# Performance work log

Hardware: AMD Instinct MI355X
Metric: run time of the kernel (lower is better)

Reference implementation:

```python
import jax, jax.numpy as jnp
import numpy as np

H = 1024          # hidden_size
A = 8             # num_actions
T = 64            # timesteps
N = 256           # batch (num envs)


def _gru_cell(x, h, Wih, Whh, bih, bhh):
    # torch.nn.GRUCell math; gate order (r, z, n)
    gi = x @ Wih.T + bih           # [N, 3H]
    gh = h @ Whh.T + bhh           # [N, 3H]
    i_r, i_z, i_n = jnp.split(gi, 3, axis=1)
    h_r, h_z, h_n = jnp.split(gh, 3, axis=1)
    r = jax.nn.sigmoid(i_r + h_r)
    z = jax.nn.sigmoid(i_z + h_z)
    n = jnp.tanh(i_n + r * h_n)
    return (1.0 - z) * n + z * h


def setup_inputs() -> dict:
    key = jax.random.key(0)
    ks = jax.random.split(key, 12)
    s = 0.02
    return {
        "c": jax.random.normal(ks[0], (T * N, H), jnp.float32),
        "hxs": jax.random.normal(ks[1], (N, 3 * H), jnp.float32),
        "masks": jnp.ones((T * N, 1), jnp.float32),
        "prev_action_one_hot": jnp.zeros((T * N, A), jnp.float32).at[jnp.arange(T * N), jax.random.randint(ks[2], (T * N,), 0, A)].set(1.0),
        "h_gru_Wih": s * jax.random.normal(ks[3], (3 * H, H), jnp.float32),
        "h_gru_Whh": s * jax.random.normal(ks[4], (3 * H, H), jnp.float32),
        "h_gru_bih": jnp.zeros((3 * H,), jnp.float32),
        "h_gru_bhh": jnp.zeros((3 * H,), jnp.float32),
        "f_gru_Wih": s * jax.random.normal(ks[5], (3 * H, H), jnp.float32),
        "f_gru_Whh": s * jax.random.normal(ks[6], (3 * H, H), jnp.float32),
        "f_gru_bih": jnp.zeros((3 * H,), jnp.float32),
        "f_gru_bhh": jnp.zeros((3 * H,), jnp.float32),
        "p_W": s * jax.random.normal(ks[7], (2 * H, 2 * H + A), jnp.float32),
        "p_b": jnp.zeros((2 * H,), jnp.float32),
        "q_W": s * jax.random.normal(ks[8], (2 * H, 2 * H + A), jnp.float32),
        "q_b": jnp.zeros((2 * H,), jnp.float32),
    }


def reference(c, hxs, masks, prev_action_one_hot,
              h_gru_Wih, h_gru_Whh, h_gru_bih, h_gru_bhh,
              f_gru_Wih, f_gru_Whh, f_gru_bih, f_gru_bhh,
              p_W, p_b, q_W, q_b):
    c3 = c.reshape(T, N, H)
    m3 = masks.reshape(T, N, 1)
    a3 = prev_action_one_hot.reshape(T, N, A)
    f0 = hxs[:, :H]
    h0 = hxs[:, H:2 * H]
    q0 = hxs[:, 2 * H:]

    def step(carry, xs):
        f, h, q_mu = carry
        c_t, m_t, a_t = xs
        p_in = jnp.concatenate([h, q_mu, a_t], axis=1) * m_t
        p_dist = p_in @ p_W.T + p_b                     # [N, 2H]
        p_mu = p_dist[:, :H]
        q_in = jnp.concatenate([f, c_t, a_t], axis=1) * m_t
        q_dist = q_in @ q_W.T + q_b                     # [N, 2H]
        q_mu_new = q_dist[:, :H]
        f_new = _gru_cell(c_t, f * m_t, f_gru_Wih, f_gru_Whh, f_gru_bih, f_gru_bhh)
        h_new = _gru_cell(p_mu, h * m_t, h_gru_Wih, h_gru_Whh, h_gru_bih, h_gru_bhh)
        return (f_new, h_new, q_mu_new), (p_dist, q_dist)

    (f, h, q_mu), (p_all, q_all) = jax.lax.scan(step, (f0, h0, q0), (c3, m3, a3))
    acc_p = p_all.reshape(T * N, 2 * H)
    acc_q = q_all.reshape(T * N, 2 * H)
    hxs_out = jnp.concatenate([f, h, q_mu], axis=1)
    return acc_p, acc_q, hxs_out
```

## Files before the change

kernel.cpp:

```cpp
#include <hip/hip_runtime.h>
#include <math.h>

typedef __attribute__((ext_vector_type(8))) __bf16 bf16x8;
typedef __attribute__((ext_vector_type(4))) float f32x4;

constexpr int H = 1024, T = 64, NB = 256, TWOH = 2048, THREEH = 3072;
constexpr long long OFF_Q  = 33554432LL;
constexpr long long OFF_HX = 67108864LL;
constexpr int LA = 6;

constexpr int R_PWH = 0, R_PWQ = 2048, R_QWF = 4096, R_QWC = 6144,
              R_FWIH = 8192, R_FWHH = 11264, R_HWIH = 14336, R_HWHH = 17408;

#define LD4(p) (*reinterpret_cast<const float4*>(p))

__device__ __forceinline__ float sigf(float x) { return 1.0f / (1.0f + expf(-x)); }

__device__ __forceinline__ void gload16(const void* g, void* l) {
    __builtin_amdgcn_global_load_lds(
        (const __attribute__((address_space(1))) uint32_t*)g,
        (__attribute__((address_space(3))) uint32_t*)l, 16, 0, 0);
}

__device__ __forceinline__ void st_bf_swz(__bf16* base, int n, int k, float v) {
    base[(size_t)n * 1024 + (((k >> 3) ^ (n & 7)) << 3) + (k & 7)] = (__bf16)v;
}

#define FRAGOFF(rloc, gl) (((rloc) << 7) + ((((gl)) ^ ((rloc) & 7)) << 4))

template<int RT>
__device__ __forceinline__ void stage_tile(const char* g, char* l, int kb, int tid) {
    #pragma unroll
    for (int i = 0; i < RT / 32; ++i) {
        const int L = i * 4096 + tid * 16;
        gload16(g + (size_t)(L >> 7) * 2048 + (size_t)kb * 128 + (L & 127), l + L);
    }
}

__device__ __forceinline__ void mm128(
    int tid, char* sA, char* sB,
    const char* A, const char* B, int nit,
    f32x4 (&acc)[2][4])
{
    const int lane = tid & 63, w = tid >> 6;
    const int l15 = lane & 15, lg = lane >> 4;
    const int wr = w >> 1, wc = w & 1;
    int aoff[2][2], boff[4][2];
    #pragma unroll
    for (int fr = 0; fr < 2; ++fr)
        #pragma unroll
        for (int kk = 0; kk < 2; ++kk)
            aoff[fr][kk] = FRAGOFF(wr * 32 + fr * 16 + l15, kk * 4 + lg);
    #pragma unroll
    for (int fc = 0; fc < 4; ++fc)
        #pragma unroll
        for (int kk = 0; kk < 2; ++kk)
            boff[fc][kk] = FRAGOFF(wc * 64 + fc * 16 + l15, kk * 4 + lg);

    stage_tile<64>(A, sA, 0, tid);
    stage_tile<128>(B, sB, 0, tid);
    if (nit > 1) {
        stage_tile<64>(A, sA + 8192, 1, tid);
        stage_tile<128>(B, sB + 16384, 1, tid);
    }
    for (int kb = 0; kb < nit; ++kb) {
        const int kn = kb + 2;
        if (kn < nit) {
            const int bo = kn % 3;
            stage_tile<64>(A, sA + bo * 8192, kn, tid);
            stage_tile<128>(B, sB + bo * 16384, kn, tid);
            asm volatile("s_waitcnt vmcnt(12)" ::: "memory");
        } else if (kb + 1 < nit) {
            asm volatile("s_waitcnt vmcnt(6)" ::: "memory");
        } else {
            asm volatile("s_waitcnt vmcnt(0)" ::: "memory");
        }
        __builtin_amdgcn_s_barrier();
        __builtin_amdgcn_sched_barrier(0);
        const int bc = kb % 3;
        char* Ab = sA + bc * 8192;
        char* Bb = sB + bc * 16384;
        bf16x8 af[2][2], bv[4][2];
        #pragma unroll
        for (int fr = 0; fr < 2; ++fr)
            #pragma unroll
            for (int kk = 0; kk < 2; ++kk)
                af[fr][kk] = *reinterpret_cast<const bf16x8*>(Ab + aoff[fr][kk]);
        #pragma unroll
        for (int fc = 0; fc < 4; ++fc)
            #pragma unroll
            for (int kk = 0; kk < 2; ++kk)
                bv[fc][kk] = *reinterpret_cast<const bf16x8*>(Bb + boff[fc][kk]);
        __builtin_amdgcn_s_setprio(1);
        #pragma unroll
        for (int kk = 0; kk < 2; ++kk)
            #pragma unroll
            for (int fr = 0; fr < 2; ++fr)
                #pragma unroll
                for (int fc = 0; fc < 4; ++fc)
                    acc[fr][fc] = __builtin_amdgcn_mfma_f32_16x16x32_bf16(
                        af[fr][kk], bv[fc][kk], acc[fr][fc], 0, 0, 0);
        __builtin_amdgcn_s_setprio(0);
        __builtin_amdgcn_s_barrier();
        __builtin_amdgcn_sched_barrier(0);
    }
}

__device__ __forceinline__ void mm32g1(
    int tid, char* sA, char* sB,
    const char* A, const char* Bg,
    f32x4 (&aR)[2], f32x4 (&aZ)[2], f32x4 (&aN)[2])
{
    const int lane = tid & 63, w = tid >> 6;
    const int l15 = lane & 15, lg = lane >> 4;
    const int wr = w >> 1, wc = w & 1;
    int aoff[2], boff[2][2];
    #pragma unroll
    for (int kk = 0; kk < 2; ++kk)
        aoff[kk] = FRAGOFF(wr * 16 + l15, kk * 4 + lg);
    #pragma unroll
    for (int fc = 0; fc < 2; ++fc)
        #pragma unroll
        for (int kk = 0; kk < 2; ++kk)
            boff[fc][kk] = FRAGOFF(wc * 32 + fc * 16 + l15, kk * 4 + lg);

    auto stg = [&](int buf, int kb) {
        stage_tile<32>(A, sA + buf * 4096, kb, tid);
        #pragma unroll
        for (int g = 0; g < 3; ++g)
            stage_tile<64>(Bg + (size_t)g * 2097152, sB + buf * 24576 + g * 8192, kb, tid);
    };
    stg(0, 0);
    for (int kb = 0; kb < 16; ++kb) {
        if (kb + 1 < 16) {
            stg((kb + 1) & 1, kb + 1);
            asm volatile("s_waitcnt vmcnt(7)" ::: "memory");
        } else {
            asm volatile("s_waitcnt vmcnt(0)" ::: "memory");
        }
        __builtin_amdgcn_s_barrier();
        __builtin_amdgcn_sched_barrier(0);
        char* Ab = sA + (kb & 1) * 4096;
        char* Bb = sB + (kb & 1) * 24576;
        bf16x8 af[2];
        #pragma unroll
        for (int kk = 0; kk < 2; ++kk)
            af[kk] = *reinterpret_cast<const bf16x8*>(Ab + aoff[kk]);
        bf16x8 bvr[2][2], bvz[2][2], bvn[2][2];
        #pragma unroll
        for (int fc = 0; fc < 2; ++fc)
            #pragma unroll
            for (int kk = 0; kk < 2; ++kk) {
                bvr[fc][kk] = *reinterpret_cast<const bf16x8*>(Bb + boff[fc][kk]);
                bvz[fc][kk] = *reinterpret_cast<const bf16x8*>(Bb + 8192 + boff[fc][kk]);
                bvn[fc][kk] = *reinterpret_cast<const bf16x8*>(Bb + 16384 + boff[fc][kk]);
            }
        __builtin_amdgcn_s_setprio(1);
        #pragma unroll
        for (int kk = 0; kk < 2; ++kk)
            #pragma unroll
            for (int fc = 0; fc < 2; ++fc) {
                aR[fc] = __builtin_amdgcn_mfma_f32_16x16x32_bf16(af[kk], bvr[fc][kk], aR[fc], 0, 0, 0);
                aZ[fc] = __builtin_amdgcn_mfma_f32_16x16x32_bf16(af[kk], bvz[fc][kk], aZ[fc], 0, 0, 0);
                aN[fc] = __builtin_amdgcn_mfma_f32_16x16x32_bf16(af[kk], bvn[fc][kk], aN[fc], 0, 0, 0);
            }
        __builtin_amdgcn_s_setprio(0);
        __builtin_amdgcn_s_barrier();
        __builtin_amdgcn_sched_barrier(0);
    }
}

__device__ __forceinline__ void do_xq(int slice, int i, int tid, char* sA, char* sB,
    const char* cbfB, const char* Wb, const float* act, const float* qW, float* out)
{
    const int lane = tid & 63, w = tid >> 6;
    const int l15 = lane & 15, lg = lane >> 4;
    const int wr = w >> 1, wc = w & 1;
    const int row0 = (i >> 4) * 64, col0 = (i & 15) * 128;
    const size_t grow0 = (size_t)slice * NB + row0;
    f32x4 acc[2][4] = {};
    mm128(tid, sA, sB, cbfB + grow0 * 2048, Wb + (size_t)(R_QWC + col0) * 2048, 16, acc);
    #pragma unroll
    for (int fc = 0; fc < 4; ++fc) {
        const int gc = col0 + wc * 64 + fc * 16 + l15;
        const float* wp = qW + (size_t)gc * 2056 + 2048;
        float4 x0 = LD4(wp), x1 = LD4(wp + 4);
        #pragma unroll
        for (int fr = 0; fr < 2; ++fr)
            #pragma unroll
            for (int j = 0; j < 4; ++j) {
                const size_t n = grow0 + wr * 32 + fr * 16 + lg * 4 + j;
                const float* ar = act + n * 8;
                float4 a0 = LD4(ar), a1 = LD4(ar + 4);
                float dot = a0.x * x0.x + a0.y * x0.y + a0.z * x0.z + a0.w * x0.w
                          + a1.x * x1.x + a1.y * x1.y + a1.z * x1.z + a1.w * x1.w;
                out[OFF_Q + n * TWOH + gc] = acc[fr][fc][j] + dot;
            }
    }
}

__device__ __forceinline__ void do_gf(int slice, int i, int tid, char* sA, char* sB,
    const char* cbfB, const char* Wb, __bf16* Gfb)
{
    const int lane = tid & 63, w = tid >> 6;
    const int l15 = lane & 15, lg = lane >> 4;
    const int wr = w >> 1, wc = w & 1;
    const int row0 = (i / 24) * 64, col0 = (i % 24) * 128;
    f32x4 acc[2][4] = {};
    mm128(tid, sA, sB, cbfB + ((size_t)slice * NB + row0) * 2048,
          Wb + (size_t)(R_FWIH + col0) * 2048, 16, acc);
    __bf16* gdst = Gfb + (size_t)(slice & 7) * NB * THREEH;
    #pragma unroll
    for (int fc = 0; fc < 4; ++fc) {
        const int gc = col0 + wc * 64 + fc * 16 + l15;
        #pragma unroll
        for (int fr = 0; fr < 2; ++fr)
            #pragma unroll
            for (int j = 0; j < 4; ++j) {
                const int n = row0 + wr * 32 + fr * 16 + lg * 4 + j;
                gdst[(size_t)n * THREEH + gc] = (__bf16)acc[fr][fc][j];
            }
    }
}

__device__ __forceinline__ void do_pq(int tt, int i, int tid, char* sA, char* sB,
    const __bf16* qmu_t, const char* Wb, const float* masks, const float* act,
    const float* pW, const float* pb, float* out)
{
    const int lane = tid & 63, w = tid >> 6;
    const int l15 = lane & 15, lg = lane >> 4;
    const int wr = w >> 1, wc = w & 1;
    const int row0 = (i >> 4) * 64, col0 = (i & 15) * 128;
    f32x4 acc[2][4] = {};
    mm128(tid, sA, sB, (const char*)qmu_t + (size_t)row0 * 2048,
          Wb + (size_t)(R_PWQ + col0) * 2048, 16, acc);
    const float* mrow = masks + (size_t)tt * NB;
    float* ob = out + (size_t)tt * NB * TWOH;
    #pragma unroll
    for (int fc = 0; fc < 4; ++fc) {
        const int gc = col0 + wc * 64 + fc * 16 + l15;
        const float* wp = pW + (size_t)gc * 2056 + 2048;
        float4 x0 = LD4(wp), x1 = LD4(wp + 4);
        const float bb = pb[gc];
        #pragma unroll
        for (int fr = 0; fr < 2; ++fr)
            #pragma unroll
            for (int j = 0; j < 4; ++j) {
                const int n = row0 + wr * 32 + fr * 16 + lg * 4 + j;
                const float* ar = act + ((size_t)tt * NB + n) * 8;
                float4 a0 = LD4(ar), a1 = LD4(ar + 4);
                float dot = a0.x * x0.x + a0.y * x0.y + a0.z * x0.z + a0.w * x0.w
                          + a1.x * x1.x + a1.y * x1.y + a1.z * x1.z + a1.w * x1.w;
                ob[(size_t)n * TWOH + gc] = acc[fr][fc][j] + mrow[n] * dot + bb;
            }
    }
}

__global__ __launch_bounds__(256) void wcvt_k(
    const float* __restrict__ pW, const float* __restrict__ qW,
    const float* __restrict__ fWih, const float* __restrict__ fWhh,
    const float* __restrict__ hWih, const float* __restrict__ hWhh,
    __bf16* __restrict__ Wbf)
{
    const long i = (long)blockIdx.x * 256 + threadIdx.x;
    const int row = (int)(i >> 7);
    const int G   = (int)i & 127;
    const float* src; int stride; int koff = 0; int r;
    if (row < 2048)       { src = pW;   stride = 2056; koff = 0;    r = row; }
    else if (row < 4096)  { src = pW;   stride = 2056; koff = 1024; r = row - 2048; }
    else if (row < 6144)  { src = qW;   stride = 2056; koff = 0;    r = row - 4096; }
    else if (row < 8192)  { src = qW;   stride = 2056; koff = 1024; r = row - 6144; }
    else if (row < 11264) { src = fWih; stride = 1024; r = row - 8192; }
    else if (row < 14336) { src = fWhh; stride = 1024; r = row - 11264; }
    else if (row < 17408) { src = hWih; stride = 1024; r = row - 14336; }
    else                  { src = hWhh; stride = 1024; r = row - 17408; }
    const float* p = src + (long)r * stride + koff + G * 8;
    float4 a = LD4(p), b = LD4(p + 4);
    bf16x8 v;
    v[0] = (__bf16)a.x; v[1] = (__bf16)a.y; v[2] = (__bf16)a.z; v[3] = (__bf16)a.w;
    v[4] = (__bf16)b.x; v[5] = (__bf16)b.y; v[6] = (__bf16)b.z; v[7] = (__bf16)b.w;
    *reinterpret_cast<bf16x8*>(Wbf + (size_t)row * 1024 + ((G ^ (row & 7)) << 3)) = v;
}

__global__ __launch_bounds__(256) void ccvt_k(const float* __restrict__ c,
                                              __bf16* __restrict__ cbf) {
    const long i = (long)blockIdx.x * 256 + threadIdx.x;
    const int row = (int)(i >> 7);
    const int G   = (int)i & 127;
    const float* p = c + (size_t)row * 1024 + G * 8;
    float4 a = LD4(p), b = LD4(p + 4);
    bf16x8 v;
    v[0] = (__bf16)a.x; v[1] = (__bf16)a.y; v[2] = (__bf16)a.z; v[3] = (__bf16)a.w;
    v[4] = (__bf16)b.x; v[5] = (__bf16)b.y; v[6] = (__bf16)b.z; v[7] = (__bf16)b.w;
    *reinterpret_cast<bf16x8*>(cbf + (size_t)row * 1024 + ((G ^ (row & 7)) << 3)) = v;
}

__global__ __launch_bounds__(256) void init2_k(
    const float* __restrict__ hxs, const float* __restrict__ masks,
    float* __restrict__ fst0, float* __restrict__ hst0,
    __bf16* __restrict__ fbm0, __bf16* __restrict__ hbm0, __bf16* __restrict__ qmub0)
{
    const int idx = blockIdx.x * 256 + threadIdx.x;
    const int arr = idx >> 15;
    const int g   = idx & 32767;
    const int n   = g >> 7;
    const int G   = g & 127;
    const float m0 = masks[n];
    const float* p = hxs + (size_t)n * THREEH + arr * 1024 + G * 8;
    float4 a = LD4(p), b = LD4(p + 4);
    __bf16* dstB = arr == 0 ? fbm0 : (arr == 1 ? hbm0 : qmub0);
    bf16x8 v;
    v[0] = (__bf16)(a.x * m0); v[1] = (__bf16)(a.y * m0);
    v[2] = (__bf16)(a.z * m0); v[3] = (__bf16)(a.w * m0);
    v[4] = (__bf16)(b.x * m0); v[5] = (__bf16)(b.y * m0);
    v[6] = (__bf16)(b.z * m0); v[7] = (__bf16)(b.w * m0);
    *reinterpret_cast<bf16x8*>(dstB + (size_t)n * 1024 + ((G ^ (n & 7)) << 3)) = v;
    if (arr < 2) {
        float* dstF = arr == 0 ? fst0 : hst0;
        *reinterpret_cast<float4*>(dstF + (size_t)n * 1024 + G * 8) = a;
        *reinterpret_cast<float4*>(dstF + (size_t)n * 1024 + G * 8 + 4) = b;
    }
}

__global__ __launch_bounds__(256) void pre_k(
    const char* __restrict__ cbfB, const char* __restrict__ Wb,
    const float* __restrict__ act, const float* __restrict__ qW,
    const __bf16* __restrict__ qmb0, const float* __restrict__ masks,
    const float* __restrict__ pW, const float* __restrict__ pb,
    __bf16* __restrict__ Gfb, float* __restrict__ out)
{
    __shared__ char smem[73728];
    if (blockIdx.x < LA * 160) {
        const int s = blockIdx.x / 160;
        const int i = blockIdx.x % 160;
        if (i < 64) do_xq(s, i, threadIdx.x, smem, smem + 24576, cbfB, Wb, act, qW, out);
        else        do_gf(s, i - 64, threadIdx.x, smem, smem + 24576, cbfB, Wb, Gfb);
    } else {
        do_pq(0, blockIdx.x - LA * 160, threadIdx.x, smem, smem + 24576,
              qmb0, Wb, masks, act, pW, pb, out);
    }
}

__global__ __launch_bounds__(256) void k1_k(
    int t,
    const __bf16* __restrict__ hbm, const __bf16* __restrict__ fbm,
    __bf16* __restrict__ qmubN,
    const float* __restrict__ masks, const float* __restrict__ act,
    const float* __restrict__ qb, const float* __restrict__ qW,
    const char* __restrict__ Wb,
    __bf16* __restrict__ pmub, float* __restrict__ Shh,
    const __bf16* __restrict__ Gfb,
    const float* __restrict__ fbih, const float* __restrict__ fbhh,
    const float* __restrict__ fstF, float* __restrict__ fstN, __bf16* __restrict__ fbmN,
    float* __restrict__ out)
{
    __shared__ char smem[73728];
    char* sA = smem;
    char* sB = smem + 24576;
    const int tid = threadIdx.x;
    const int lane = tid & 63, w = tid >> 6;
    const int l15 = lane & 15, lg = lane >> 4;
    const int wr = w >> 1, wc = w & 1;
    const float* mrow = masks + (size_t)t * NB;
    const float* mn   = masks + (size_t)(t + 1 < T ? t + 1 : t) * NB;
    int b = blockIdx.x;

    if (b < 64) {
        const int row0 = (b >> 4) * 64, col0 = (b & 15) * 128;
        f32x4 acc[2][4] = {};
        mm128(tid, sA, sB,
              (const char*)hbm + (size_t)row0 * 2048,
              Wb + (size_t)(R_PWH + col0) * 2048, 16, acc);
        float* ob = out + (size_t)t * NB * TWOH;
        #pragma unroll
        for (int fc = 0; fc < 4; ++fc) {
            const int gc = col0 + wc * 64 + fc * 16 + l15;
            #pragma unroll
            for (int fr = 0; fr < 2; ++fr)
                #pragma unroll
                for (int j = 0; j < 4; ++j) {
                    const int n = row0 + wr * 32 + fr * 16 + lg * 4 + j;
                    const float v = ob[(size_t)n * TWOH + gc] + acc[fr][fc][j];
                    ob[(size_t)n * TWOH + gc] = v;
                    if (gc < 1024) st_bf_swz(pmub, n, gc, v);
                }
        }
    } else if (b < 128) {
        b -= 64;
        const int row0 = (b >> 4) * 64, col0 = (b & 15) * 128;
        f32x4 acc[2][4] = {};
        mm128(tid, sA, sB,
              (const char*)fbm + (size_t)row0 * 2048,
              Wb + (size_t)(R_QWF + col0) * 2048, 16, acc);
        float* ob = out + OFF_Q + (size_t)t * NB * TWOH;
        #pragma unroll
        for (int fc = 0; fc < 4; ++fc) {
            const int gc = col0 + wc * 64 + fc * 16 + l15;
            const float bb = qb[gc];
            #pragma unroll
            for (int fr = 0; fr < 2; ++fr)
                #pragma unroll
                for (int j = 0; j < 4; ++j) {
                    const int n = row0 + wr * 32 + fr * 16 + lg * 4 + j;
                    const float xq = ob[(size_t)n * TWOH + gc];
                    float v = acc[fr][fc][j] + mrow[n] * xq + bb;
                    ob[(size_t)n * TWOH + gc] = v;
                    if (gc < 1024) st_bf_swz(qmubN, n, gc, v * mn[n]);
                }
        }
    } else if (b < 224) {
        const int i = b - 128;
        const int row0 = (i / 24) * 64, col0 = (i % 24) * 128;
        f32x4 acc[2][4] = {};
        mm128(tid, sA, sB,
              (const char*)hbm + (size_t)row0 * 2048,
              Wb + (size_t)(R_HWHH + col0) * 2048, 16, acc);
        #pragma unroll
        for (int fc = 0; fc < 4; ++fc) {
            const int gc = col0 + wc * 64 + fc * 16 + l15;
            #pragma unroll
            for (int fr = 0; fr < 2; ++fr)
                #pragma unroll
                for (int j = 0; j < 4; ++j) {
                    const int n = row0 + wr * 32 + fr * 16 + lg * 4 + j;
                    Shh[(size_t)n * THREEH + gc] = acc[fr][fc][j];
                }
        }
    } else {
        const int i = b - 224;
        const int row0 = (i >> 4) * 32, col0 = (i & 15) * 64;
        f32x4 aR[2] = {}, aZ[2] = {}, aN[2] = {};
        mm32g1(tid, sA, sB,
               (const char*)fbm + (size_t)row0 * 2048,
               Wb + (size_t)(R_FWHH + col0) * 2048, aR, aZ, aN);
        const __bf16* gsl = Gfb + (size_t)(t & 7) * NB * THREEH;
        #pragma unroll
        for (int fc = 0; fc < 2; ++fc) {
            const int col = col0 + wc * 32 + fc * 16 + l15;
            const float br  = fbih[col] + fbhh[col];
            const float bz  = fbih[col + 1024] + fbhh[col + 1024];
            const float bni = fbih[col + 2048], bnh = fbhh[col + 2048];
            #pragma unroll
            for (int j = 0; j < 4; ++j) {
                const int n = row0 + wr * 16 + lg * 4 + j;
                const float gfr = (float)gsl[(size_t)n * THREEH + col];
                const float gfz = (float)gsl[(size_t)n * THREEH + col + 1024];
                const float gfn = (float)gsl[(size_t)n * THREEH + col + 2048];
                const float rg = sigf(gfr + aR[fc][j] + br);
                const float zg = sigf(gfz + aZ[fc][j] + bz);
                const float ng = tanhf(gfn + bni + rg * (aN[fc][j] + bnh));
                const float fm = fstF[(size_t)n * 1024 + col] * mrow[n];
                const float o = (1.f - zg) * ng + zg * fm;
                fstN[(size_t)n * 1024 + col] = o;
                st_bf_swz(fbmN, n, col, o * mn[n]);
            }
        }
    }
}

__global__ __launch_bounds__(256) void k2_k(
    int t,
    const __bf16* __restrict__ pmub, const __bf16* __restrict__ qmubN,
    const char* __restrict__ cbfB,
    const float* __restrict__ Shh,
    const float* __restrict__ hstF, float* __restrict__ hstN, __bf16* __restrict__ hbmN,
    const char* __restrict__ Wb,
    const float* __restrict__ hbih, const float* __restrict__ hbhh,
    const float* __restrict__ masks, const float* __restrict__ act,
    const float* __restrict__ pW, const float* __restrict__ pb,
    const float* __restrict__ qW,
    __bf16* __restrict__ Gfb, float* __restrict__ out)
{
    __shared__ char smem[73728];
    char* sA = smem;
    char* sB = smem + 24576;
    const int tid = threadIdx.x;
    const int lane = tid & 63, w = tid >> 6;
    const int l15 = lane & 15, lg = lane >> 4;
    const int wr = w >> 1, wc = w & 1;
    const float* mrow = masks + (size_t)t * NB;
    const float* mn   = masks + (size_t)(t + 1 < T ? t + 1 : t) * NB;
    const int b = blockIdx.x;

    if (b < 128) {
        const int row0 = (b >> 4) * 32, col0 = (b & 15) * 64;
        f32x4 aR[2] = {}, aZ[2] = {}, aN[2] = {};
        mm32g1(tid, sA, sB,
               (const char*)pmub + (size_t)row0 * 2048,
               Wb + (size_t)(R_HWIH + col0) * 2048, aR, aZ, aN);
        #pragma unroll
        for (int fc = 0; fc < 2; ++fc) {
            const int col = col0 + wc * 32 + fc * 16 + l15;
            const float bri = hbih[col],        brh = hbhh[col];
            const float bzi = hbih[col + 1024], bzh = hbhh[col + 1024];
            const float bni = hbih[col + 2048], bnh = hbhh[col + 2048];
            #pragma unroll
            for (int j = 0; j < 4; ++j) {
                const int n = row0 + wr * 16 + lg * 4 + j;
                const float ghr = Shh[(size_t)n * THREEH + col];
                const float ghz = Shh[(size_t)n * THREEH + col + 1024];
                const float ghn = Shh[(size_t)n * THREEH + col + 2048];
                const float rg = sigf(aR[fc][j] + bri + ghr + brh);
                const float zg = sigf(aZ[fc][j] + bzi + ghz + bzh);
                const float ng = tanhf(aN[fc][j] + bni + rg * (ghn + bnh));
                const float hm = hstF[(size_t)n * 1024 + col] * mrow[n];
                const float o = (1.f - zg) * ng + zg * hm;
                hstN[(size_t)n * 1024 + col] = o;
                st_bf_swz(hbmN, n, col, o * mn[n]);
            }
        }
    } else if (b < 192) {
        if (t + 1 < T)
            do_pq(t + 1, b - 128, tid, sA, sB, qmubN, Wb, masks, act, pW, pb, out);
    } else if (b < 256) {
        if (t + LA < T)
            do_xq(t + LA, b - 192, tid, sA, sB, cbfB, Wb, act, qW, out);
    } else {
        if (t + LA < T)
            do_gf(t + LA, b - 256, tid, sA, sB, cbfB, Wb, Gfb);
    }
}

__global__ __launch_bounds__(256) void write_hxs_k(const float* __restrict__ fS,
                                                   const float* __restrict__ hS,
                                                   float* out) {
    const int i = blockIdx.x * 256 + threadIdx.x;
    const int n = i / THREEH;
    const int j = i - n * THREEH;
    float v;
    if (j < H)          v = fS[(size_t)n * H + j];
    else if (j < TWOH)  v = hS[(size_t)n * H + (j - H)];
    else                v = out[OFF_Q + ((size_t)(T - 1) * NB + n) * TWOH + (j - TWOH)];
    out[OFF_HX + i] = v;
}

extern "C" void kernel_launch(void* const* d_in, const int* in_sizes, int n_in,
                              void* d_out, int out_size, void* d_ws, size_t ws_size,
                              hipStream_t stream) {
    (void)in_sizes; (void)n_in; (void)out_size; (void)ws_size;

    const float* c     = (const float*)d_in[0];
    const float* hxs   = (const float*)d_in[1];
    const float* masks = (const float*)d_in[2];
    const float* act   = (const float*)d_in[3];
    const float* hWih  = (const float*)d_in[4];
    const float* hWhh  = (const float*)d_in[5];
    const float* hbih  = (const float*)d_in[6];
    const float* hbhh  = (const float*)d_in[7];
    const float* fWih  = (const float*)d_in[8];
    const float* fWhh  = (const float*)d_in[9];
    const float* fbih  = (const float*)d_in[10];
    const float* fbhh  = (const float*)d_in[11];
    const float* pW    = (const float*)d_in[12];
    const float* pb    = (const float*)d_in[13];
    const float* qW    = (const float*)d_in[14];
    const float* qb    = (const float*)d_in[15];

    float* out = (float*)d_out;
    char*  wsb = (char*)d_ws;

    __bf16* Wbf  = (__bf16*)(wsb);
    __bf16* cbf  = (__bf16*)(wsb + 41943040LL);
    float*  fst[2] = { (float*)(wsb + 75497472LL), (float*)(wsb + 76546048LL) };
    float*  hst[2] = { (float*)(wsb + 77594624LL), (float*)(wsb + 78643200LL) };
    __bf16* fbm[2] = { (__bf16*)(wsb + 79691776LL), (__bf16*)(wsb + 80216064LL) };
    __bf16* hbm[2] = { (__bf16*)(wsb + 80740352LL), (__bf16*)(wsb + 81264640LL) };
    __bf16* qmb[2] = { (__bf16*)(wsb + 81788928LL), (__bf16*)(wsb + 82313216LL) };
    __bf16* pmub   = (__bf16*)(wsb + 82837504LL);
    float*  Shh    = (float*)(wsb + 83361792LL);
    __bf16* Gfb    = (__bf16*)(wsb + 86507520LL);
    const char* Wb   = (const char*)Wbf;
    const char* cbfB = (const char*)cbf;

    wcvt_k <<<dim3(10240), dim3(256), 0, stream>>>(pW, qW, fWih, fWhh, hWih, hWhh, Wbf);
    ccvt_k <<<dim3(8192),  dim3(256), 0, stream>>>(c, cbf);
    init2_k<<<dim3(384),   dim3(256), 0, stream>>>(hxs, masks, fst[0], hst[0],
                                                   fbm[0], hbm[0], qmb[0]);
    pre_k  <<<dim3(LA * 160 + 64), dim3(256), 0, stream>>>(
        cbfB, Wb, act, qW, qmb[0], masks, pW, pb, Gfb, out);

    for (int t = 0; t < T; ++t) {
        const int cur = t & 1, nxt = cur ^ 1;
        k1_k<<<dim3(352), dim3(256), 0, stream>>>(
            t, hbm[cur], fbm[cur], qmb[nxt],
            masks, act, qb, qW, Wb, pmub, Shh, Gfb,
            fbih, fbhh, fst[cur], fst[nxt], fbm[nxt], out);
        k2_k<<<dim3(352), dim3(256), 0, stream>>>(
            t, pmub, qmb[nxt], cbfB, Shh,
            hst[cur], hst[nxt], hbm[nxt],
            Wb, hbih, hbhh, masks, act, pW, pb, qW, Gfb, out);
    }

    write_hxs_k<<<dim3(3072), dim3(256), 0, stream>>>(fst[0], hst[0], out);
}
```

Baseline: 2.107 ms.

## Load weight B-fragments straight from global into registers, dropping LDS staging

The GEMM helpers now read weight fragments directly from global memory into a double-buffered register set, using unswizzled weight rows. Only the activation tile still goes through a triple-buffered LDS ring. This shrinks shared memory from 72KB to 24KB per block, which allows more resident blocks and removes LDS write/read traffic for the weights. In exchange it uses more VGPRs and issues uncoalesced-ish per-lane global loads for B, which could expose latency.

```diff
diff --git a/kernel.cpp b/kernel.cpp
--- a/kernel.cpp
+++ b/kernel.cpp
@@ -38,59 +38,56 @@
 }
 
 __device__ __forceinline__ void mm128(
-    int tid, char* sA, char* sB,
-    const char* A, const char* B, int nit,
+    int tid, char* sA,
+    const char* A, const char* B,
     f32x4 (&acc)[2][4])
 {
     const int lane = tid & 63, w = tid >> 6;
     const int l15 = lane & 15, lg = lane >> 4;
     const int wr = w >> 1, wc = w & 1;
-    int aoff[2][2], boff[4][2];
+    int aoff[2][2];
     #pragma unroll
     for (int fr = 0; fr < 2; ++fr)
         #pragma unroll
         for (int kk = 0; kk < 2; ++kk)
             aoff[fr][kk] = FRAGOFF(wr * 32 + fr * 16 + l15, kk * 4 + lg);
+    const char* Bp[4];
     #pragma unroll
     for (int fc = 0; fc < 4; ++fc)
+        Bp[fc] = B + (size_t)(wc * 64 + fc * 16 + l15) * 2048 + (lg << 4);
+
+    bf16x8 br0[4][2], br1[4][2];
+    stage_tile<64>(A, sA, 0, tid);
+    stage_tile<64>(A, sA + 8192, 1, tid);
+    #pragma unroll
+    for (int fc = 0; fc < 4; ++fc)
         #pragma unroll
         for (int kk = 0; kk < 2; ++kk)
-            boff[fc][kk] = FRAGOFF(wc * 64 + fc * 16 + l15, kk * 4 + lg);
-
-    stage_tile<64>(A, sA, 0, tid);
-    stage_tile<128>(B, sB, 0, tid);
-    if (nit > 1) {
-        stage_tile<64>(A, sA + 8192, 1, tid);
-        stage_tile<128>(B, sB + 16384, 1, tid);
-    }
-    for (int kb = 0; kb < nit; ++kb) {
-        const int kn = kb + 2;
-        if (kn < nit) {
-            const int bo = kn % 3;
-            stage_tile<64>(A, sA + bo * 8192, kn, tid);
-            stage_tile<128>(B, sB + bo * 16384, kn, tid);
-            asm volatile("s_waitcnt vmcnt(12)" ::: "memory");
-        } else if (kb + 1 < nit) {
-            asm volatile("s_waitcnt vmcnt(6)" ::: "memory");
-        } else {
-            asm volatile("s_waitcnt vmcnt(0)" ::: "memory");
-        }
+            br0[fc][kk] = *reinterpret_cast<const bf16x8*>(Bp[fc] + kk * 64);
+
+    auto step = [&](int kb, bf16x8 (&bc)[4][2], bf16x8 (&bw)[4][2]) {
+        if (kb + 2 < 16)
+            stage_tile<64>(A, sA + ((kb + 2) % 3) * 8192, kb + 2, tid);
+        if (kb + 1 < 16) {
+            #pragma unroll
+            for (int fc = 0; fc < 4; ++fc)
+                #pragma unroll
+                for (int kk = 0; kk < 2; ++kk)
+                    bw[fc][kk] = *reinterpret_cast<const bf16x8*>(
+                        Bp[fc] + (kb + 1) * 128 + kk * 64);
+        }
+        if (kb + 2 < 16)      asm volatile("s_waitcnt vmcnt(10)" ::: "memory");
+        else if (kb + 1 < 16) asm volatile("s_waitcnt vmcnt(8)" ::: "memory");
+        else                  asm volatile("s_waitcnt vmcnt(0)" ::: "memory");
         __builtin_amdgcn_s_barrier();
         __builtin_amdgcn_sched_barrier(0);
-        const int bc = kb % 3;
-        char* Ab = sA + bc * 8192;
-        char* Bb = sB + bc * 16384;
-        bf16x8 af[2][2], bv[4][2];
+        char* Ab = sA + (kb % 3) * 8192;
+        bf16x8 af[2][2];
         #pragma unroll
         for (int fr = 0; fr < 2; ++fr)
             #pragma unroll
             for (int kk = 0; kk < 2; ++kk)
                 af[fr][kk] = *reinterpret_cast<const bf16x8*>(Ab + aoff[fr][kk]);
-        #pragma unroll
-        for (int fc = 0; fc < 4; ++fc)
-            #pragma unroll
-            for (int kk = 0; kk < 2; ++kk)
-                bv[fc][kk] = *reinterpret_cast<const bf16x8*>(Bb + boff[fc][kk]);
         __builtin_amdgcn_s_setprio(1);
         #pragma unroll
         for (int kk = 0; kk < 2; ++kk)
@@ -99,78 +96,93 @@
                 #pragma unroll
                 for (int fc = 0; fc < 4; ++fc)
                     acc[fr][fc] = __builtin_amdgcn_mfma_f32_16x16x32_bf16(
-                        af[fr][kk], bv[fc][kk], acc[fr][fc], 0, 0, 0);
+                        af[fr][kk], bc[fc][kk], acc[fr][fc], 0, 0, 0);
         __builtin_amdgcn_s_setprio(0);
         __builtin_amdgcn_s_barrier();
         __builtin_amdgcn_sched_barrier(0);
+    };
+    #pragma unroll
+    for (int k2 = 0; k2 < 8; ++k2) {
+        step(2 * k2,     br0, br1);
+        step(2 * k2 + 1, br1, br0);
     }
 }
 
 __device__ __forceinline__ void mm32g1(
-    int tid, char* sA, char* sB,
+    int tid, char* sA,
     const char* A, const char* Bg,
     f32x4 (&aR)[2], f32x4 (&aZ)[2], f32x4 (&aN)[2])
 {
     const int lane = tid & 63, w = tid >> 6;
     const int l15 = lane & 15, lg = lane >> 4;
     const int wr = w >> 1, wc = w & 1;
-    int aoff[2], boff[2][2];
+    int aoff[2];
     #pragma unroll
     for (int kk = 0; kk < 2; ++kk)
         aoff[kk] = FRAGOFF(wr * 16 + l15, kk * 4 + lg);
-    #pragma unroll
-    for (int fc = 0; fc < 2; ++fc)
-        #pragma unroll
-        for (int kk = 0; kk < 2; ++kk)
-            boff[fc][kk] = FRAGOFF(wc * 32 + fc * 16 + l15, kk * 4 + lg);
-
-    auto stg = [&](int buf, int kb) {
-        stage_tile<32>(A, sA + buf * 4096, kb, tid);
-        #pragma unroll
-        for (int g = 0; g < 3; ++g)
-            stage_tile<64>(Bg + (size_t)g * 2097152, sB + buf * 24576 + g * 8192, kb, tid);
-    };
-    stg(0, 0);
-    for (int kb = 0; kb < 16; ++kb) {
+    const char* Bp[3][2];
+    #pragma unroll
+    for (int g = 0; g < 3; ++g)
+        #pragma unroll
+        for (int fc = 0; fc < 2; ++fc)
+            Bp[g][fc] = Bg + (size_t)g * 2097152
+                        + (size_t)(wc * 32 + fc * 16 + l15) * 2048 + (lg << 4);
+
+    bf16x8 br0[3][2][2], br1[3][2][2];
+    stage_tile<32>(A, sA, 0, tid);
+    stage_tile<32>(A, sA + 4096, 1, tid);
+    #pragma unroll
+    for (int g = 0; g < 3; ++g)
+        #pragma unroll
+        for (int fc = 0; fc < 2; ++fc)
+            #pragma unroll
+            for (int kk = 0; kk < 2; ++kk)
+                br0[g][fc][kk] = *reinterpret_cast<const bf16x8*>(Bp[g][fc] + kk * 64);
+
+    auto step = [&](int kb, bf16x8 (&bc)[3][2][2], bf16x8 (&bw)[3][2][2]) {
+        if (kb + 2 < 16)
+            stage_tile<32>(A, sA + ((kb + 2) % 3) * 4096, kb + 2, tid);
         if (kb + 1 < 16) {
-            stg((kb + 1) & 1, kb + 1);
-            asm volatile("s_waitcnt vmcnt(7)" ::: "memory");
-        } else {
-            asm volatile("s_waitcnt vmcnt(0)" ::: "memory");
-        }
+            #pragma unroll
+            for (int g = 0; g < 3; ++g)
+                #pragma unroll
+                for (int fc = 0; fc < 2; ++fc)
+                    #pragma unroll
+                    for (int kk = 0; kk < 2; ++kk)
+                        bw[g][fc][kk] = *reinterpret_cast<const bf16x8*>(
+                            Bp[g][fc] + (kb + 1) * 128 + kk * 64);
+        }
+        if (kb + 2 < 16)      asm volatile("s_waitcnt vmcnt(13)" ::: "memory");
+        else if (kb + 1 < 16) asm volatile("s_waitcnt vmcnt(12)" ::: "memory");
+        else                  asm volatile("s_waitcnt vmcnt(0)" ::: "memory");
         __builtin_amdgcn_s_barrier();
         __builtin_amdgcn_sched_barrier(0);
-        char* Ab = sA + (kb & 1) * 4096;
-        char* Bb = sB + (kb & 1) * 24576;
+        char* Ab = sA + (kb % 3) * 4096;
         bf16x8 af[2];
         #pragma unroll
         for (int kk = 0; kk < 2; ++kk)
             af[kk] = *reinterpret_cast<const bf16x8*>(Ab + aoff[kk]);
-        bf16x8 bvr[2][2], bvz[2][2], bvn[2][2];
-        #pragma unroll
-        for (int fc = 0; fc < 2; ++fc)
-            #pragma unroll
-            for (int kk = 0; kk < 2; ++kk) {
-                bvr[fc][kk] = *reinterpret_cast<const bf16x8*>(Bb + boff[fc][kk]);
-                bvz[fc][kk] = *reinterpret_cast<const bf16x8*>(Bb + 8192 + boff[fc][kk]);
-                bvn[fc][kk] = *reinterpret_cast<const bf16x8*>(Bb + 16384 + boff[fc][kk]);
-            }
         __builtin_amdgcn_s_setprio(1);
         #pragma unroll
         for (int kk = 0; kk < 2; ++kk)
             #pragma unroll
             for (int fc = 0; fc < 2; ++fc) {
-                aR[fc] = __builtin_amdgcn_mfma_f32_16x16x32_bf16(af[kk], bvr[fc][kk], aR[fc], 0, 0, 0);
-                aZ[fc] = __builtin_amdgcn_mfma_f32_16x16x32_bf16(af[kk], bvz[fc][kk], aZ[fc], 0, 0, 0);
-                aN[fc] = __builtin_amdgcn_mfma_f32_16x16x32_bf16(af[kk], bvn[fc][kk], aN[fc], 0, 0, 0);
+                aR[fc] = __builtin_amdgcn_mfma_f32_16x16x32_bf16(af[kk], bc[0][fc][kk], aR[fc], 0, 0, 0);
+                aZ[fc] = __builtin_amdgcn_mfma_f32_16x16x32_bf16(af[kk], bc[1][fc][kk], aZ[fc], 0, 0, 0);
+                aN[fc] = __builtin_amdgcn_mfma_f32_16x16x32_bf16(af[kk], bc[2][fc][kk], aN[fc], 0, 0, 0);
             }
         __builtin_amdgcn_s_setprio(0);
         __builtin_amdgcn_s_barrier();
         __builtin_amdgcn_sched_barrier(0);
-    }
-}
-
-__device__ __forceinline__ void do_xq(int slice, int i, int tid, char* sA, char* sB,
+    };
+    #pragma unroll
+    for (int k2 = 0; k2 < 8; ++k2) {
+        step(2 * k2,     br0, br1);
+        step(2 * k2 + 1, br1, br0);
+    }
+}
+
+__device__ __forceinline__ void do_xq(int slice, int i, int tid, char* sA,
     const char* cbfB, const char* Wb, const float* act, const float* qW, float* out)
 {
     const int lane = tid & 63, w = tid >> 6;
@@ -179,7 +191,7 @@
     const int row0 = (i >> 4) * 64, col0 = (i & 15) * 128;
     const size_t grow0 = (size_t)slice * NB + row0;
     f32x4 acc[2][4] = {};
-    mm128(tid, sA, sB, cbfB + grow0 * 2048, Wb + (size_t)(R_QWC + col0) * 2048, 16, acc);
+    mm128(tid, sA, cbfB + grow0 * 2048, Wb + (size_t)(R_QWC + col0) * 2048, acc);
     #pragma unroll
     for (int fc = 0; fc < 4; ++fc) {
         const int gc = col0 + wc * 64 + fc * 16 + l15;
@@ -199,7 +211,7 @@
     }
 }
 
-__device__ __forceinline__ void do_gf(int slice, int i, int tid, char* sA, char* sB,
+__device__ __forceinline__ void do_gf(int slice, int i, int tid, char* sA,
     const char* cbfB, const char* Wb, __bf16* Gfb)
 {
     const int lane = tid & 63, w = tid >> 6;
@@ -207,8 +219,8 @@
     const int wr = w >> 1, wc = w & 1;
     const int row0 = (i / 24) * 64, col0 = (i % 24) * 128;
     f32x4 acc[2][4] = {};
-    mm128(tid, sA, sB, cbfB + ((size_t)slice * NB + row0) * 2048,
-          Wb + (size_t)(R_FWIH + col0) * 2048, 16, acc);
+    mm128(tid, sA, cbfB + ((size_t)slice * NB + row0) * 2048,
+          Wb + (size_t)(R_FWIH + col0) * 2048, acc);
     __bf16* gdst = Gfb + (size_t)(slice & 7) * NB * THREEH;
     #pragma unroll
     for (int fc = 0; fc < 4; ++fc) {
@@ -223,7 +235,7 @@
     }
 }
 
-__device__ __forceinline__ void do_pq(int tt, int i, int tid, char* sA, char* sB,
+__device__ __forceinline__ void do_pq(int tt, int i, int tid, char* sA,
     const __bf16* qmu_t, const char* Wb, const float* masks, const float* act,
     const float* pW, const float* pb, float* out)
 {
@@ -232,8 +244,8 @@
     const int wr = w >> 1, wc = w & 1;
     const int row0 = (i >> 4) * 64, col0 = (i & 15) * 128;
     f32x4 acc[2][4] = {};
-    mm128(tid, sA, sB, (const char*)qmu_t + (size_t)row0 * 2048,
-          Wb + (size_t)(R_PWQ + col0) * 2048, 16, acc);
+    mm128(tid, sA, (const char*)qmu_t + (size_t)row0 * 2048,
+          Wb + (size_t)(R_PWQ + col0) * 2048, acc);
     const float* mrow = masks + (size_t)tt * NB;
     float* ob = out + (size_t)tt * NB * TWOH;
     #pragma unroll
@@ -279,7 +291,7 @@
     bf16x8 v;
     v[0] = (__bf16)a.x; v[1] = (__bf16)a.y; v[2] = (__bf16)a.z; v[3] = (__bf16)a.w;
     v[4] = (__bf16)b.x; v[5] = (__bf16)b.y; v[6] = (__bf16)b.z; v[7] = (__bf16)b.w;
-    *reinterpret_cast<bf16x8*>(Wbf + (size_t)row * 1024 + ((G ^ (row & 7)) << 3)) = v;
+    *reinterpret_cast<bf16x8*>(Wbf + (size_t)row * 1024 + G * 8) = v;
 }
 
 __global__ __launch_bounds__(256) void ccvt_k(const float* __restrict__ c,
@@ -329,15 +341,15 @@
     const float* __restrict__ pW, const float* __restrict__ pb,
     __bf16* __restrict__ Gfb, float* __restrict__ out)
 {
-    __shared__ char smem[73728];
-    if (blockIdx.x < LA * 160) {
-        const int s = blockIdx.x / 160;
-        const int i = blockIdx.x % 160;
-        if (i < 64) do_xq(s, i, threadIdx.x, smem, smem + 24576, cbfB, Wb, act, qW, out);
-        else        do_gf(s, i - 64, threadIdx.x, smem, smem + 24576, cbfB, Wb, Gfb);
+    __shared__ char smem[24576];
+    const int b = blockIdx.x;
+    if (b < LA * 160) {
+        const int s = b / 160;
+        const int i = b % 160;
+        if (i < 64) do_xq(s, i, threadIdx.x, smem, cbfB, Wb, act, qW, out);
+        else        do_gf(s, i - 64, threadIdx.x, smem, cbfB, Wb, Gfb);
     } else {
-        do_pq(0, blockIdx.x - LA * 160, threadIdx.x, smem, smem + 24576,
-              qmb0, Wb, masks, act, pW, pb, out);
+        do_pq(0, b - LA * 160, threadIdx.x, smem, qmb0, Wb, masks, act, pW, pb, out);
     }
 }
 
@@ -354,9 +366,7 @@
     const float* __restrict__ fstF, float* __restrict__ fstN, __bf16* __restrict__ fbmN,
     float* __restrict__ out)
 {
-    __shared__ char smem[73728];
-    char* sA = smem;
-    char* sB = smem + 24576;
+    __shared__ char smem[24576];
     const int tid = threadIdx.x;
     const int lane = tid & 63, w = tid >> 6;
     const int l15 = lane & 15, lg = lane >> 4;
@@ -368,9 +378,8 @@
     if (b < 64) {
         const int row0 = (b >> 4) * 64, col0 = (b & 15) * 128;
         f32x4 acc[2][4] = {};
-        mm128(tid, sA, sB,
-              (const char*)hbm + (size_t)row0 * 2048,
-              Wb + (size_t)(R_PWH + col0) * 2048, 16, acc);
+        mm128(tid, smem, (const char*)hbm + (size_t)row0 * 2048,
+              Wb + (size_t)(R_PWH + col0) * 2048, acc);
         float* ob = out + (size_t)t * NB * TWOH;
         #pragma unroll
         for (int fc = 0; fc < 4; ++fc) {
@@ -389,9 +398,8 @@
         b -= 64;
         const int row0 = (b >> 4) * 64, col0 = (b & 15) * 128;
         f32x4 acc[2][4] = {};
-        mm128(tid, sA, sB,
-              (const char*)fbm + (size_t)row0 * 2048,
-              Wb + (size_t)(R_QWF + col0) * 2048, 16, acc);
+        mm128(tid, smem, (const char*)fbm + (size_t)row0 * 2048,
+              Wb + (size_t)(R_QWF + col0) * 2048, acc);
         float* ob = out + OFF_Q + (size_t)t * NB * TWOH;
         #pragma unroll
         for (int fc = 0; fc < 4; ++fc) {
@@ -412,9 +420,8 @@
         const int i = b - 128;
         const int row0 = (i / 24) * 64, col0 = (i % 24) * 128;
         f32x4 acc[2][4] = {};
-        mm128(tid, sA, sB,
-              (const char*)hbm + (size_t)row0 * 2048,
-              Wb + (size_t)(R_HWHH + col0) * 2048, 16, acc);
+        mm128(tid, smem, (const char*)hbm + (size_t)row0 * 2048,
+              Wb + (size_t)(R_HWHH + col0) * 2048, acc);
         #pragma unroll
         for (int fc = 0; fc < 4; ++fc) {
             const int gc = col0 + wc * 64 + fc * 16 + l15;
@@ -430,8 +437,7 @@
         const int i = b - 224;
         const int row0 = (i >> 4) * 32, col0 = (i & 15) * 64;
         f32x4 aR[2] = {}, aZ[2] = {}, aN[2] = {};
-        mm32g1(tid, sA, sB,
-               (const char*)fbm + (size_t)row0 * 2048,
+        mm32g1(tid, smem, (const char*)fbm + (size_t)row0 * 2048,
                Wb + (size_t)(R_FWHH + col0) * 2048, aR, aZ, aN);
         const __bf16* gsl = Gfb + (size_t)(t & 7) * NB * THREEH;
         #pragma unroll
@@ -471,9 +477,7 @@
     const float* __restrict__ qW,
     __bf16* __restrict__ Gfb, float* __restrict__ out)
 {
-    __shared__ char smem[73728];
-    char* sA = smem;
-    char* sB = smem + 24576;
+    __shared__ char smem[24576];
     const int tid = threadIdx.x;
     const int lane = tid & 63, w = tid >> 6;
     const int l15 = lane & 15, lg = lane >> 4;
@@ -485,8 +489,7 @@
     if (b < 128) {
         const int row0 = (b >> 4) * 32, col0 = (b & 15) * 64;
         f32x4 aR[2] = {}, aZ[2] = {}, aN[2] = {};
-        mm32g1(tid, sA, sB,
-               (const char*)pmub + (size_t)row0 * 2048,
+        mm32g1(tid, smem, (const char*)pmub + (size_t)row0 * 2048,
                Wb + (size_t)(R_HWIH + col0) * 2048, aR, aZ, aN);
         #pragma unroll
         for (int fc = 0; fc < 2; ++fc) {
@@ -511,13 +514,13 @@
         }
     } else if (b < 192) {
         if (t + 1 < T)
-            do_pq(t + 1, b - 128, tid, sA, sB, qmubN, Wb, masks, act, pW, pb, out);
+            do_pq(t + 1, b - 128, tid, smem, qmubN, Wb, masks, act, pW, pb, out);
     } else if (b < 256) {
         if (t + LA < T)
-            do_xq(t + LA, b - 192, tid, sA, sB, cbfB, Wb, act, qW, out);
+            do_xq(t + LA, b - 192, tid, smem, cbfB, Wb, act, qW, out);
     } else {
         if (t + LA < T)
-            do_gf(t + LA, b - 256, tid, sA, sB, cbfB, Wb, Gfb);
+            do_gf(t + LA, b - 256, tid, smem, cbfB, Wb, Gfb);
     }
 }
 
```

Result: slower. 5.565 ms (+164.1%).
